# Optimization experiments

Hardware: AMD Instinct MI355X
Metric: run time of the kernel (lower is better)

## Reference

```python
import jax, jax.numpy as jnp
import numpy as np

NUM_HEADS = 8
EPS = 1e-12  # torch F.normalize default eps


def _l2_normalize(t, axis):
    n = jnp.sqrt(jnp.sum(t * t, axis=axis, keepdims=True))
    return t / jnp.maximum(n, EPS)


def setup_inputs() -> dict:
    key = jax.random.key(0)
    k1, k2, k3 = jax.random.split(key, 3)
    B, N, D = 32, 3136, 384
    x = jax.random.normal(k1, (B, N, D), dtype=jnp.float32)
    qkv_w = jax.random.normal(k2, (3 * D, D), dtype=jnp.float32) * (1.0 / np.sqrt(D))
    temperature = jnp.ones((NUM_HEADS, 1, 1), dtype=jnp.float32)
    proj_w = jax.random.normal(k3, (D, D), dtype=jnp.float32) * (1.0 / np.sqrt(D))
    proj_b = jnp.zeros((D,), dtype=jnp.float32)
    return {"x": x, "qkv_w": qkv_w, "temperature": temperature,
            "proj_w": proj_w, "proj_b": proj_b}


def reference(x, qkv_w, temperature, proj_w, proj_b):
    B, N, D = x.shape
    H = NUM_HEADS
    C = D // H
    # qkv projection (no bias), split last dim as (3, H, C) -> (3, B, H, C, N)
    qkv = jnp.einsum('bnd,ed->bne', x, qkv_w)
    qkv = qkv.reshape(B, N, 3, H, C).transpose(2, 0, 3, 4, 1)
    q, k, v = qkv[0], qkv[1], qkv[2]            # each (B, H, C, N)
    q = _l2_normalize(q, axis=-1)               # normalize over tokens N
    k = _l2_normalize(k, axis=-1)
    # cross-covariance attention: (B, H, C, C), scaled by per-head temperature
    attn = jnp.einsum('bhcn,bhdn->bhcd', q, k) * temperature
    attn = jax.nn.softmax(attn, axis=-1)
    out = jnp.einsum('bhcd,bhdn->bhcn', attn, v)  # (B, H, C, N)
    out = out.transpose(0, 3, 1, 2).reshape(B, N, D)
    return jnp.einsum('bnd,ed->bne', out, proj_w) + proj_b
```

## Files before the change

kernel.cpp:

```cpp
#include <hip/hip_runtime.h>


typedef __bf16 bf16x8 __attribute__((ext_vector_type(8)));
typedef float floatx4 __attribute__((ext_vector_type(4)));
typedef unsigned short u16;

#define B_ 32
#define N_ 3136
#define D_ 384
#define H_ 8
#define C_ 48
#define E3_ 1152
#define BN_ 100352

__device__ __forceinline__ u16 f2b(float f) {
  unsigned u = __builtin_bit_cast(unsigned, f);
  u += 0x7FFFu + ((u >> 16) & 1u);
  return (u16)(u >> 16);
}
__device__ __forceinline__ void gload16(const u16* g, u16* l) {
  __builtin_amdgcn_global_load_lds(
      (const __attribute__((address_space(1))) void*)g,
      (__attribute__((address_space(3))) void*)l, 16, 0, 0);
}

__global__ __launch_bounds__(256) void k_cvt(const float* __restrict__ in,
                                             u16* __restrict__ out, int n4) {
  int i = blockIdx.x * 256 + threadIdx.x;
  if (i < n4) {
    float4 v = ((const float4*)in)[i];
    ushort4 o;
    o.x = f2b(v.x); o.y = f2b(v.y); o.z = f2b(v.z); o.w = f2b(v.w);
    ((ushort4*)out)[i] = o;
  }
}

__global__ __launch_bounds__(256) void k_gemm_qkv(const u16* __restrict__ W,
                                                  const u16* __restrict__ X,
                                                  u16* __restrict__ O) {
  const int K = D_;
  int lin = blockIdx.y * 9 + blockIdx.x;
  int w = (lin & 7) * 882 + (lin >> 3);
  int m0 = (w % 9) * 128;
  int n0 = (w / 9) * 128;
  __shared__ u16 As[2][128][32];
  __shared__ u16 Bs[2][128][32];
  int t = threadIdx.x, wid = t >> 6, lane = t & 63;
  int srow = wid * 32 + (lane >> 2);
  int scol = (lane & 3) * 8;
  int wm = (wid & 1) * 64, wn = (wid >> 1) * 64;
  int r = lane & 15, quad = lane >> 4, q8 = quad * 8;

  const u16* gA = W + (size_t)(m0 + srow) * K + scol;
  const u16* gB = X + (size_t)(n0 + srow) * K + scol;

  floatx4 acc[4][4] = {};
  for (int k0 = 0; k0 < K; k0 += 64) {
#pragma unroll
    for (int ks = 0; ks < 2; ks++) {
      gload16(gA + k0 + ks * 32,          &As[ks][wid * 32][0]);
      gload16(gA + k0 + ks * 32 + 16 * K, &As[ks][wid * 32 + 16][0]);
      gload16(gB + k0 + ks * 32,          &Bs[ks][wid * 32][0]);
      gload16(gB + k0 + ks * 32 + 16 * K, &Bs[ks][wid * 32 + 16][0]);
    }
    __syncthreads();
#pragma unroll
    for (int ks = 0; ks < 2; ks++) {
      bf16x8 af[4], bf[4];
#pragma unroll
      for (int i = 0; i < 4; i++) af[i] = *(const bf16x8*)(&As[ks][wm + i * 16 + r][q8]);
#pragma unroll
      for (int j = 0; j < 4; j++) bf[j] = *(const bf16x8*)(&Bs[ks][wn + j * 16 + r][q8]);
#pragma unroll
      for (int i = 0; i < 4; i++)
#pragma unroll
        for (int j = 0; j < 4; j++)
          acc[i][j] = __builtin_amdgcn_mfma_f32_16x16x32_bf16(af[i], bf[j], acc[i][j], 0, 0, 0);
    }
    __syncthreads();
  }
#pragma unroll
  for (int i = 0; i < 4; i++)
#pragma unroll
    for (int j = 0; j < 4; j++)
#pragma unroll
      for (int v = 0; v < 4; v++) {
        int rr = m0 + wm + i * 16 + quad * 4 + v;
        int cc = n0 + wn + j * 16 + r;
        O[(size_t)rr * BN_ + cc] = f2b(acc[i][j][v]);
      }
}

__global__ __launch_bounds__(256) void k_attn_s(const u16* __restrict__ QKV,
                                                float* __restrict__ S,
                                                float* __restrict__ ssq) {
  int bh = blockIdx.x, b = bh >> 3, h = bh & 7;
  int ns = blockIdx.y * 448;
  const u16* Qb = QKV + (size_t)(h * C_) * BN_ + b * N_ + ns;
  const u16* Kb = QKV + (size_t)(D_ + h * C_) * BN_ + b * N_ + ns;
  __shared__ u16 As[64][32];
  __shared__ u16 Bs[64][32];
  int t = threadIdx.x, wid = t >> 6, lane = t & 63;
  int wm = (wid & 1) * 32, wn = (wid >> 1) * 32;
  int r = lane & 15, quad = lane >> 4, q8 = quad * 8;
  int srow = wid * 16 + (lane >> 2);
  int scol = (lane & 3) * 8;
  const u16* gQ = Qb + (size_t)srow * BN_ + scol;
  const u16* gK = Kb + (size_t)srow * BN_ + scol;
  u16* lQ = &As[wid * 16][0];
  u16* lK = &Bs[wid * 16][0];

  floatx4 acc[2][2] = {};
  floatx4 dq0 = {}, dq1 = {}, dk0 = {}, dk1 = {};
  for (int k0 = 0; k0 < 448; k0 += 32) {
    gload16(gQ + k0, lQ);
    gload16(gK + k0, lK);
    __syncthreads();
    bf16x8 a0 = *(const bf16x8*)(&As[wm + r][q8]);
    bf16x8 a1 = *(const bf16x8*)(&As[wm + 16 + r][q8]);
    bf16x8 b0 = *(const bf16x8*)(&Bs[wn + r][q8]);
    bf16x8 b1 = *(const bf16x8*)(&Bs[wn + 16 + r][q8]);
    acc[0][0] = __builtin_amdgcn_mfma_f32_16x16x32_bf16(a0, b0, acc[0][0], 0, 0, 0);
    acc[0][1] = __builtin_amdgcn_mfma_f32_16x16x32_bf16(a0, b1, acc[0][1], 0, 0, 0);
    acc[1][0] = __builtin_amdgcn_mfma_f32_16x16x32_bf16(a1, b0, acc[1][0], 0, 0, 0);
    acc[1][1] = __builtin_amdgcn_mfma_f32_16x16x32_bf16(a1, b1, acc[1][1], 0, 0, 0);
    if (wid == 0) {
      dq0 = __builtin_amdgcn_mfma_f32_16x16x32_bf16(a0, a0, dq0, 0, 0, 0);
      dq1 = __builtin_amdgcn_mfma_f32_16x16x32_bf16(a1, a1, dq1, 0, 0, 0);
      dk0 = __builtin_amdgcn_mfma_f32_16x16x32_bf16(b0, b0, dk0, 0, 0, 0);
      dk1 = __builtin_amdgcn_mfma_f32_16x16x32_bf16(b1, b1, dk1, 0, 0, 0);
    } else if (wid == 1) {
      dq0 = __builtin_amdgcn_mfma_f32_16x16x32_bf16(a0, a0, dq0, 0, 0, 0);
    } else if (wid == 2) {
      dk0 = __builtin_amdgcn_mfma_f32_16x16x32_bf16(b0, b0, dk0, 0, 0, 0);
    }
    __syncthreads();
  }
#pragma unroll
  for (int v = 0; v < 4; v++) {
    if (r == quad * 4 + v) {
      int dr = quad * 4 + v;
      if (wid == 0) {
        atomicAdd(&ssq[bh * 48 + dr],              dq0[v]);
        atomicAdd(&ssq[bh * 48 + 16 + dr],         dq1[v]);
        atomicAdd(&ssq[12288 + bh * 48 + dr],      dk0[v]);
        atomicAdd(&ssq[12288 + bh * 48 + 16 + dr], dk1[v]);
      } else if (wid == 1) {
        atomicAdd(&ssq[bh * 48 + 32 + dr], dq0[v]);
      } else if (wid == 2) {
        atomicAdd(&ssq[12288 + bh * 48 + 32 + dr], dk0[v]);
      }
    }
  }
#pragma unroll
  for (int mt = 0; mt < 2; mt++)
#pragma unroll
    for (int nt = 0; nt < 2; nt++)
#pragma unroll
      for (int v = 0; v < 4; v++) {
        int rr = wm + mt * 16 + quad * 4 + v;
        int cc = wn + nt * 16 + r;
        if (rr < 48 && cc < 48)
          atomicAdd(&S[(size_t)bh * 2304 + rr * 48 + cc], acc[mt][nt][v]);
      }
}

__global__ __launch_bounds__(64) void k_softmax(const float* __restrict__ S,
                                                const float* __restrict__ ssq,
                                                const float* __restrict__ temp,
                                                u16* __restrict__ attnb) {
  int bh = blockIdx.x, h = bh & 7;
  int c = threadIdx.x;
  if (c >= 48) return;
  float sq = 1.f / fmaxf(sqrtf(ssq[bh * 48 + c]), 1e-12f);
  float T = temp[h];
  const float* Srow = S + (size_t)bh * 2304 + c * 48;
  float v[48];
  float mx = -1e30f;
#pragma unroll
  for (int d = 0; d < 48; d++) {
    float sk = 1.f / fmaxf(sqrtf(ssq[12288 + bh * 48 + d]), 1e-12f);
    float l = Srow[d] * sq * sk * T;
    v[d] = l;
    mx = fmaxf(mx, l);
  }
  float sum = 0.f;
#pragma unroll
  for (int d = 0; d < 48; d++) { v[d] = expf(v[d] - mx); sum += v[d]; }
  float inv = 1.f / sum;
  u16* Arow = attnb + (size_t)bh * 3072 + c * 64;
#pragma unroll
  for (int d = 0; d < 48; d++) Arow[d] = f2b(v[d] * inv);
#pragma unroll
  for (int d = 48; d < 64; d++) Arow[d] = 0;
}

__global__ __launch_bounds__(256) void k_attn_v(const u16* __restrict__ QKV,
                                                const u16* __restrict__ attnb,
                                                u16* __restrict__ outT) {
  int bh = blockIdx.y, b = bh >> 3, h = bh & 7;
  int n0 = blockIdx.x * 64;
  const u16* V = QKV + (size_t)(2 * D_ + h * C_) * BN_ + b * N_;
  __shared__ u16 Vt[64][64];
  __shared__ u16 Aw[48][64];
  int t = threadIdx.x;
  for (int i = t; i < 512; i += 256) ((int4*)Vt)[i] = int4{0, 0, 0, 0};
  {
    const int4* src = (const int4*)(attnb + (size_t)bh * 3072);
    for (int i = t; i < 384; i += 256) ((int4*)Aw)[i] = src[i];
  }
  __syncthreads();
  for (int idx = t; idx < 768; idx += 256) {
    int d = idx >> 4, c4 = (idx & 15) * 4;
    ushort4 v = *(const ushort4*)(V + (size_t)d * BN_ + n0 + c4);
    Vt[c4 + 0][d] = v.x; Vt[c4 + 1][d] = v.y;
    Vt[c4 + 2][d] = v.z; Vt[c4 + 3][d] = v.w;
  }
  __syncthreads();
  int wid = t >> 6, lane = t & 63;
  int r = lane & 15, quad = lane >> 4, q8 = quad * 8;
  floatx4 acc[3] = {};
#pragma unroll
  for (int ks = 0; ks < 2; ks++) {
    bf16x8 a = *(const bf16x8*)(&Vt[wid * 16 + r][ks * 32 + q8]);
#pragma unroll
    for (int nt = 0; nt < 3; nt++) {
      bf16x8 bb = *(const bf16x8*)(&Aw[nt * 16 + r][ks * 32 + q8]);
      acc[nt] = __builtin_amdgcn_mfma_f32_16x16x32_bf16(a, bb, acc[nt], 0, 0, 0);
    }
  }
  u16* Ob = outT + (size_t)(b * N_) * D_;
#pragma unroll
  for (int nt = 0; nt < 3; nt++)
#pragma unroll
    for (int j = 0; j < 4; j++) {
      int n = n0 + wid * 16 + quad * 4 + j;
      int e = h * C_ + nt * 16 + r;
      Ob[(size_t)n * D_ + e] = f2b(acc[nt][j]);
    }
}

__global__ __launch_bounds__(256) void k_gemm_proj(const u16* __restrict__ OT,
                                                   const u16* __restrict__ P,
                                                   const float* __restrict__ bias,
                                                   float* __restrict__ Y) {
  const int K = D_;
  int lin = blockIdx.y * 3 + blockIdx.x;
  int w = (lin & 7) * 294 + (lin >> 3);
  int n0 = (w % 3) * 128;
  int m0 = (w / 3) * 128;
  __shared__ u16 As[2][128][32];
  __shared__ u16 Bs[2][128][32];
  int t = threadIdx.x, wid = t >> 6, lane = t & 63;
  int srow = wid * 32 + (lane >> 2);
  int scol = (lane & 3) * 8;
  int wm = (wid & 1) * 64, wn = (wid >> 1) * 64;
  int r = lane & 15, quad = lane >> 4, q8 = quad * 8;

  const u16* gA = OT + (size_t)(m0 + srow) * K + scol;
  const u16* gB = P + (size_t)(n0 + srow) * K + scol;

  floatx4 acc[4][4] = {};
  for (int k0 = 0; k0 < K; k0 += 64) {
#pragma unroll
    for (int ks = 0; ks < 2; ks++) {
      gload16(gA + k0 + ks * 32,          &As[ks][wid * 32][0]);
      gload16(gA + k0 + ks * 32 + 16 * K, &As[ks][wid * 32 + 16][0]);
      gload16(gB + k0 + ks * 32,          &Bs[ks][wid * 32][0]);
      gload16(gB + k0 + ks * 32 + 16 * K, &Bs[ks][wid * 32 + 16][0]);
    }
    __syncthreads();
#pragma unroll
    for (int ks = 0; ks < 2; ks++) {
      bf16x8 af[4], bf[4];
#pragma unroll
      for (int i = 0; i < 4; i++) af[i] = *(const bf16x8*)(&As[ks][wm + i * 16 + r][q8]);
#pragma unroll
      for (int j = 0; j < 4; j++) bf[j] = *(const bf16x8*)(&Bs[ks][wn + j * 16 + r][q8]);
#pragma unroll
      for (int i = 0; i < 4; i++)
#pragma unroll
        for (int j = 0; j < 4; j++)
          acc[i][j] = __builtin_amdgcn_mfma_f32_16x16x32_bf16(af[i], bf[j], acc[i][j], 0, 0, 0);
    }
    __syncthreads();
  }
#pragma unroll
  for (int i = 0; i < 4; i++)
#pragma unroll
    for (int j = 0; j < 4; j++) {
      int cc = n0 + wn + j * 16 + r;
      float bv = bias[cc];
#pragma unroll
      for (int v = 0; v < 4; v++) {
        int rr = m0 + wm + i * 16 + quad * 4 + v;
        Y[(size_t)rr * D_ + cc] = acc[i][j][v] + bv;
      }
    }
}

extern "C" void kernel_launch(void* const* d_in, const int* in_sizes, int n_in,
                              void* d_out, int out_size, void* d_ws, size_t ws_size,
                              hipStream_t stream) {
  const float* x      = (const float*)d_in[0];
  const float* qkv_w  = (const float*)d_in[1];
  const float* temp   = (const float*)d_in[2];
  const float* proj_w = (const float*)d_in[3];
  const float* proj_b = (const float*)d_in[4];
  float* out = (float*)d_out;

  char* ws = (char*)d_ws;
  u16*   qkv    = (u16*)(ws);
  u16*   xbf    = (u16*)(ws + 231211008);
  u16*   wbf    = (u16*)(ws + 308281344);
  u16*   pwbf   = (u16*)(ws + 309166080);
  float* S      = (float*)(ws + 309460992);
  float* ssq    = (float*)(ws + 311820288);
  u16*   attnb  = (u16*)(ws + 311918592);
  u16*   outT   = xbf;

  hipMemsetAsync(S, 0, 2359296 + 98304, stream);

  k_cvt<<<38535168 / 4 / 256, 256, 0, stream>>>(x, xbf, 38535168 / 4);
  k_cvt<<<442368 / 4 / 256, 256, 0, stream>>>(qkv_w, wbf, 442368 / 4);
  k_cvt<<<147456 / 4 / 256, 256, 0, stream>>>(proj_w, pwbf, 147456 / 4);

  k_gemm_qkv<<<dim3(9, 784), 256, 0, stream>>>(wbf, xbf, qkv);
  k_attn_s<<<dim3(256, 7), 256, 0, stream>>>(qkv, S, ssq);
  k_softmax<<<256, 64, 0, stream>>>(S, ssq, temp, attnb);
  k_attn_v<<<dim3(49, 256), 256, 0, stream>>>(qkv, attnb, outT);
  k_gemm_proj<<<dim3(3, 784), 256, 0, stream>>>(outT, pwbf, proj_b, out);
}
```

Baseline: 593.4 us.

## Reassociate attention via per-batch Gram matrix to avoid materializing QKV

Rewrites the pipeline algebraically: computes the per-batch Gram matrix X^T X (384x384) once. The q·k products and the q/k norms are then derived from W G W^T, and the value projection, attention and output projection are folded into one per-batch 384x384 matrix R that multiplies x directly. This drops the large QKV activation write and read, the per-head attention-v pass and the separate projection GEMM, at the cost of an extra transposed bf16 copy of x, fp32 atomic accumulation into G, and more bf16 rounding steps (G, U and R are each rounded to bf16).

Measured after the change: 557.6 us. 6.0% less time.

```diff
diff --git a/kernel.cpp b/kernel.cpp
--- a/kernel.cpp
+++ b/kernel.cpp
@@ -10,7 +10,6 @@
 #define D_ 384
 #define H_ 8
 #define C_ 48
-#define E3_ 1152
 #define BN_ 100352
 
 __device__ __forceinline__ u16 f2b(float f) {
@@ -35,33 +34,67 @@
   }
 }
 
-__global__ __launch_bounds__(256) void k_gemm_qkv(const u16* __restrict__ W,
-                                                  const u16* __restrict__ X,
-                                                  u16* __restrict__ O) {
-  const int K = D_;
-  int lin = blockIdx.y * 9 + blockIdx.x;
-  int w = (lin & 7) * 882 + (lin >> 3);
-  int m0 = (w % 9) * 128;
-  int n0 = (w / 9) * 128;
+__global__ __launch_bounds__(256) void k_cvt_t(const float* __restrict__ x,
+                                               u16* __restrict__ xbf,
+                                               u16* __restrict__ xT) {
+  int d0 = blockIdx.x * 64, n0 = blockIdx.y * 64, b = blockIdx.z;
+  const float* xp = x + ((size_t)b * N_ + n0) * D_ + d0;
+  __shared__ u16 L[64][68];
+  int t = threadIdx.x;
+  int nl = t >> 4, dl = (t & 15) * 4;
+#pragma unroll
+  for (int p = 0; p < 4; p++) {
+    int n = nl + p * 16;
+    float4 v = *(const float4*)(xp + (size_t)n * D_ + dl);
+    ushort4 o;
+    o.x = f2b(v.x); o.y = f2b(v.y); o.z = f2b(v.z); o.w = f2b(v.w);
+    *(ushort4*)(xbf + ((size_t)(b * N_ + n0 + n)) * D_ + d0 + dl) = o;
+    *(ushort4*)(&L[n][dl]) = o;
+  }
+  __syncthreads();
+  int dl2 = t >> 4, nl2 = (t & 15) * 4;
+#pragma unroll
+  for (int p = 0; p < 4; p++) {
+    int d = dl2 + p * 16;
+    ushort4 o;
+    o.x = L[nl2 + 0][d]; o.y = L[nl2 + 1][d];
+    o.z = L[nl2 + 2][d]; o.w = L[nl2 + 3][d];
+    *(ushort4*)(xT + (size_t)(d0 + d) * BN_ + b * N_ + n0 + nl2) = o;
+  }
+}
+
+__global__ __launch_bounds__(256) void k_wvt(const float* __restrict__ qkv_w,
+                                             u16* __restrict__ wvT) {
+  int h = blockIdx.x, t = threadIdx.x;
+  for (int idx = t; idx < 384 * 64; idx += 256) {
+    int j = idx >> 6, d = idx & 63;
+    float v = (d < 48) ? qkv_w[(size_t)(2 * D_ + h * C_ + d) * D_ + j] : 0.f;
+    wvT[(size_t)h * 24576 + idx] = f2b(v);
+  }
+}
+
+__global__ __launch_bounds__(256) void k_gram(const u16* __restrict__ xT,
+                                              float* __restrict__ G) {
+  int tile = blockIdx.x, b = blockIdx.y, ns = blockIdx.z * 448;
+  int m0 = (tile % 3) * 128, n0 = (tile / 3) * 128;
   __shared__ u16 As[2][128][32];
   __shared__ u16 Bs[2][128][32];
   int t = threadIdx.x, wid = t >> 6, lane = t & 63;
-  int srow = wid * 32 + (lane >> 2);
-  int scol = (lane & 3) * 8;
+  int srow = wid * 32 + (lane >> 2), scol = (lane & 3) * 8;
   int wm = (wid & 1) * 64, wn = (wid >> 1) * 64;
   int r = lane & 15, quad = lane >> 4, q8 = quad * 8;
-
-  const u16* gA = W + (size_t)(m0 + srow) * K + scol;
-  const u16* gB = X + (size_t)(n0 + srow) * K + scol;
+  const u16* base = xT + (size_t)b * N_ + ns + scol;
+  const u16* gA = base + (size_t)(m0 + srow) * BN_;
+  const u16* gB = base + (size_t)(n0 + srow) * BN_;
 
   floatx4 acc[4][4] = {};
-  for (int k0 = 0; k0 < K; k0 += 64) {
-#pragma unroll
-    for (int ks = 0; ks < 2; ks++) {
-      gload16(gA + k0 + ks * 32,          &As[ks][wid * 32][0]);
-      gload16(gA + k0 + ks * 32 + 16 * K, &As[ks][wid * 32 + 16][0]);
-      gload16(gB + k0 + ks * 32,          &Bs[ks][wid * 32][0]);
-      gload16(gB + k0 + ks * 32 + 16 * K, &Bs[ks][wid * 32 + 16][0]);
+  for (int k0 = 0; k0 < 448; k0 += 64) {
+#pragma unroll
+    for (int ks = 0; ks < 2; ks++) {
+      gload16(gA + k0 + ks * 32,                     &As[ks][wid * 32][0]);
+      gload16(gA + k0 + ks * 32 + (size_t)16 * BN_,  &As[ks][wid * 32 + 16][0]);
+      gload16(gB + k0 + ks * 32,                     &Bs[ks][wid * 32][0]);
+      gload16(gB + k0 + ks * 32 + (size_t)16 * BN_,  &Bs[ks][wid * 32 + 16][0]);
     }
     __syncthreads();
 #pragma unroll
@@ -79,6 +112,7 @@
     }
     __syncthreads();
   }
+  float* Gb = G + (size_t)b * 147456;
 #pragma unroll
   for (int i = 0; i < 4; i++)
 #pragma unroll
@@ -87,187 +121,31 @@
       for (int v = 0; v < 4; v++) {
         int rr = m0 + wm + i * 16 + quad * 4 + v;
         int cc = n0 + wn + j * 16 + r;
-        O[(size_t)rr * BN_ + cc] = f2b(acc[i][j][v]);
-      }
-}
-
-__global__ __launch_bounds__(256) void k_attn_s(const u16* __restrict__ QKV,
-                                                float* __restrict__ S,
-                                                float* __restrict__ ssq) {
-  int bh = blockIdx.x, b = bh >> 3, h = bh & 7;
-  int ns = blockIdx.y * 448;
-  const u16* Qb = QKV + (size_t)(h * C_) * BN_ + b * N_ + ns;
-  const u16* Kb = QKV + (size_t)(D_ + h * C_) * BN_ + b * N_ + ns;
-  __shared__ u16 As[64][32];
-  __shared__ u16 Bs[64][32];
-  int t = threadIdx.x, wid = t >> 6, lane = t & 63;
-  int wm = (wid & 1) * 32, wn = (wid >> 1) * 32;
-  int r = lane & 15, quad = lane >> 4, q8 = quad * 8;
-  int srow = wid * 16 + (lane >> 2);
-  int scol = (lane & 3) * 8;
-  const u16* gQ = Qb + (size_t)srow * BN_ + scol;
-  const u16* gK = Kb + (size_t)srow * BN_ + scol;
-  u16* lQ = &As[wid * 16][0];
-  u16* lK = &Bs[wid * 16][0];
-
-  floatx4 acc[2][2] = {};
-  floatx4 dq0 = {}, dq1 = {}, dk0 = {}, dk1 = {};
-  for (int k0 = 0; k0 < 448; k0 += 32) {
-    gload16(gQ + k0, lQ);
-    gload16(gK + k0, lK);
-    __syncthreads();
-    bf16x8 a0 = *(const bf16x8*)(&As[wm + r][q8]);
-    bf16x8 a1 = *(const bf16x8*)(&As[wm + 16 + r][q8]);
-    bf16x8 b0 = *(const bf16x8*)(&Bs[wn + r][q8]);
-    bf16x8 b1 = *(const bf16x8*)(&Bs[wn + 16 + r][q8]);
-    acc[0][0] = __builtin_amdgcn_mfma_f32_16x16x32_bf16(a0, b0, acc[0][0], 0, 0, 0);
-    acc[0][1] = __builtin_amdgcn_mfma_f32_16x16x32_bf16(a0, b1, acc[0][1], 0, 0, 0);
-    acc[1][0] = __builtin_amdgcn_mfma_f32_16x16x32_bf16(a1, b0, acc[1][0], 0, 0, 0);
-    acc[1][1] = __builtin_amdgcn_mfma_f32_16x16x32_bf16(a1, b1, acc[1][1], 0, 0, 0);
-    if (wid == 0) {
-      dq0 = __builtin_amdgcn_mfma_f32_16x16x32_bf16(a0, a0, dq0, 0, 0, 0);
-      dq1 = __builtin_amdgcn_mfma_f32_16x16x32_bf16(a1, a1, dq1, 0, 0, 0);
-      dk0 = __builtin_amdgcn_mfma_f32_16x16x32_bf16(b0, b0, dk0, 0, 0, 0);
-      dk1 = __builtin_amdgcn_mfma_f32_16x16x32_bf16(b1, b1, dk1, 0, 0, 0);
-    } else if (wid == 1) {
-      dq0 = __builtin_amdgcn_mfma_f32_16x16x32_bf16(a0, a0, dq0, 0, 0, 0);
-    } else if (wid == 2) {
-      dk0 = __builtin_amdgcn_mfma_f32_16x16x32_bf16(b0, b0, dk0, 0, 0, 0);
-    }
-    __syncthreads();
-  }
-#pragma unroll
-  for (int v = 0; v < 4; v++) {
-    if (r == quad * 4 + v) {
-      int dr = quad * 4 + v;
-      if (wid == 0) {
-        atomicAdd(&ssq[bh * 48 + dr],              dq0[v]);
-        atomicAdd(&ssq[bh * 48 + 16 + dr],         dq1[v]);
-        atomicAdd(&ssq[12288 + bh * 48 + dr],      dk0[v]);
-        atomicAdd(&ssq[12288 + bh * 48 + 16 + dr], dk1[v]);
-      } else if (wid == 1) {
-        atomicAdd(&ssq[bh * 48 + 32 + dr], dq0[v]);
-      } else if (wid == 2) {
-        atomicAdd(&ssq[12288 + bh * 48 + 32 + dr], dk0[v]);
-      }
-    }
-  }
-#pragma unroll
-  for (int mt = 0; mt < 2; mt++)
-#pragma unroll
-    for (int nt = 0; nt < 2; nt++)
-#pragma unroll
-      for (int v = 0; v < 4; v++) {
-        int rr = wm + mt * 16 + quad * 4 + v;
-        int cc = wn + nt * 16 + r;
-        if (rr < 48 && cc < 48)
-          atomicAdd(&S[(size_t)bh * 2304 + rr * 48 + cc], acc[mt][nt][v]);
-      }
-}
-
-__global__ __launch_bounds__(64) void k_softmax(const float* __restrict__ S,
-                                                const float* __restrict__ ssq,
-                                                const float* __restrict__ temp,
-                                                u16* __restrict__ attnb) {
-  int bh = blockIdx.x, h = bh & 7;
-  int c = threadIdx.x;
-  if (c >= 48) return;
-  float sq = 1.f / fmaxf(sqrtf(ssq[bh * 48 + c]), 1e-12f);
-  float T = temp[h];
-  const float* Srow = S + (size_t)bh * 2304 + c * 48;
-  float v[48];
-  float mx = -1e30f;
-#pragma unroll
-  for (int d = 0; d < 48; d++) {
-    float sk = 1.f / fmaxf(sqrtf(ssq[12288 + bh * 48 + d]), 1e-12f);
-    float l = Srow[d] * sq * sk * T;
-    v[d] = l;
-    mx = fmaxf(mx, l);
-  }
-  float sum = 0.f;
-#pragma unroll
-  for (int d = 0; d < 48; d++) { v[d] = expf(v[d] - mx); sum += v[d]; }
-  float inv = 1.f / sum;
-  u16* Arow = attnb + (size_t)bh * 3072 + c * 64;
-#pragma unroll
-  for (int d = 0; d < 48; d++) Arow[d] = f2b(v[d] * inv);
-#pragma unroll
-  for (int d = 48; d < 64; d++) Arow[d] = 0;
-}
-
-__global__ __launch_bounds__(256) void k_attn_v(const u16* __restrict__ QKV,
-                                                const u16* __restrict__ attnb,
-                                                u16* __restrict__ outT) {
-  int bh = blockIdx.y, b = bh >> 3, h = bh & 7;
-  int n0 = blockIdx.x * 64;
-  const u16* V = QKV + (size_t)(2 * D_ + h * C_) * BN_ + b * N_;
-  __shared__ u16 Vt[64][64];
-  __shared__ u16 Aw[48][64];
-  int t = threadIdx.x;
-  for (int i = t; i < 512; i += 256) ((int4*)Vt)[i] = int4{0, 0, 0, 0};
-  {
-    const int4* src = (const int4*)(attnb + (size_t)bh * 3072);
-    for (int i = t; i < 384; i += 256) ((int4*)Aw)[i] = src[i];
-  }
-  __syncthreads();
-  for (int idx = t; idx < 768; idx += 256) {
-    int d = idx >> 4, c4 = (idx & 15) * 4;
-    ushort4 v = *(const ushort4*)(V + (size_t)d * BN_ + n0 + c4);
-    Vt[c4 + 0][d] = v.x; Vt[c4 + 1][d] = v.y;
-    Vt[c4 + 2][d] = v.z; Vt[c4 + 3][d] = v.w;
-  }
-  __syncthreads();
-  int wid = t >> 6, lane = t & 63;
-  int r = lane & 15, quad = lane >> 4, q8 = quad * 8;
-  floatx4 acc[3] = {};
-#pragma unroll
-  for (int ks = 0; ks < 2; ks++) {
-    bf16x8 a = *(const bf16x8*)(&Vt[wid * 16 + r][ks * 32 + q8]);
-#pragma unroll
-    for (int nt = 0; nt < 3; nt++) {
-      bf16x8 bb = *(const bf16x8*)(&Aw[nt * 16 + r][ks * 32 + q8]);
-      acc[nt] = __builtin_amdgcn_mfma_f32_16x16x32_bf16(a, bb, acc[nt], 0, 0, 0);
-    }
-  }
-  u16* Ob = outT + (size_t)(b * N_) * D_;
-#pragma unroll
-  for (int nt = 0; nt < 3; nt++)
-#pragma unroll
-    for (int j = 0; j < 4; j++) {
-      int n = n0 + wid * 16 + quad * 4 + j;
-      int e = h * C_ + nt * 16 + r;
-      Ob[(size_t)n * D_ + e] = f2b(acc[nt][j]);
-    }
-}
-
-__global__ __launch_bounds__(256) void k_gemm_proj(const u16* __restrict__ OT,
-                                                   const u16* __restrict__ P,
-                                                   const float* __restrict__ bias,
-                                                   float* __restrict__ Y) {
-  const int K = D_;
-  int lin = blockIdx.y * 3 + blockIdx.x;
-  int w = (lin & 7) * 294 + (lin >> 3);
-  int n0 = (w % 3) * 128;
-  int m0 = (w / 3) * 128;
+        atomicAdd(&Gb[(size_t)rr * 384 + cc], acc[i][j][v]);
+      }
+}
+
+__global__ __launch_bounds__(256) void k_mid1(const u16* __restrict__ wbf,
+                                              const u16* __restrict__ Gb,
+                                              float* __restrict__ U) {
+  int m0 = blockIdx.x * 128, n0 = blockIdx.y * 128, b = blockIdx.z;
   __shared__ u16 As[2][128][32];
   __shared__ u16 Bs[2][128][32];
   int t = threadIdx.x, wid = t >> 6, lane = t & 63;
-  int srow = wid * 32 + (lane >> 2);
-  int scol = (lane & 3) * 8;
+  int srow = wid * 32 + (lane >> 2), scol = (lane & 3) * 8;
   int wm = (wid & 1) * 64, wn = (wid >> 1) * 64;
   int r = lane & 15, quad = lane >> 4, q8 = quad * 8;
-
-  const u16* gA = OT + (size_t)(m0 + srow) * K + scol;
-  const u16* gB = P + (size_t)(n0 + srow) * K + scol;
+  const u16* gA = wbf + (size_t)(m0 + srow) * 384 + scol;
+  const u16* gB = Gb + (size_t)b * 147456 + (size_t)(n0 + srow) * 384 + scol;
 
   floatx4 acc[4][4] = {};
-  for (int k0 = 0; k0 < K; k0 += 64) {
-#pragma unroll
-    for (int ks = 0; ks < 2; ks++) {
-      gload16(gA + k0 + ks * 32,          &As[ks][wid * 32][0]);
-      gload16(gA + k0 + ks * 32 + 16 * K, &As[ks][wid * 32 + 16][0]);
-      gload16(gB + k0 + ks * 32,          &Bs[ks][wid * 32][0]);
-      gload16(gB + k0 + ks * 32 + 16 * K, &Bs[ks][wid * 32 + 16][0]);
+  for (int k0 = 0; k0 < 384; k0 += 64) {
+#pragma unroll
+    for (int ks = 0; ks < 2; ks++) {
+      gload16(gA + k0 + ks * 32,            &As[ks][wid * 32][0]);
+      gload16(gA + k0 + ks * 32 + 16 * 384, &As[ks][wid * 32 + 16][0]);
+      gload16(gB + k0 + ks * 32,            &Bs[ks][wid * 32][0]);
+      gload16(gB + k0 + ks * 32 + 16 * 384, &Bs[ks][wid * 32 + 16][0]);
     }
     __syncthreads();
 #pragma unroll
@@ -285,16 +163,260 @@
     }
     __syncthreads();
   }
+  float* Ub = U + (size_t)b * 294912;
 #pragma unroll
   for (int i = 0; i < 4; i++)
 #pragma unroll
-    for (int j = 0; j < 4; j++) {
-      int cc = n0 + wn + j * 16 + r;
-      float bv = bias[cc];
+    for (int j = 0; j < 4; j++)
 #pragma unroll
       for (int v = 0; v < 4; v++) {
         int rr = m0 + wm + i * 16 + quad * 4 + v;
-        Y[(size_t)rr * D_ + cc] = acc[i][j][v] + bv;
+        int cc = n0 + wn + j * 16 + r;
+        Ub[(size_t)rr * 384 + cc] = acc[i][j][v];
+      }
+}
+
+__global__ __launch_bounds__(256) void k_mid2(const float* __restrict__ U,
+                                              const u16* __restrict__ wbf,
+                                              const u16* __restrict__ wvT,
+                                              const float* __restrict__ temp,
+                                              u16* __restrict__ MT) {
+  int bh = blockIdx.x, b = bh >> 3, h = bh & 7;
+  __shared__ __align__(16) u16 sUq[48][32], sUk[48][32], sWq[48][32], sWk[48][32];
+  __shared__ __align__(16) u16 sA[48][72];
+  __shared__ float sSsq[96];
+  __shared__ float sInv[96];
+  int t = threadIdx.x, wid = t >> 6, lane = t & 63;
+  int r = lane & 15, quad = lane >> 4, q8 = quad * 8;
+  const float* Uq = U + (size_t)b * 294912 + (size_t)(h * C_) * 384;
+  const float* Uk = U + (size_t)b * 294912 + (size_t)(D_ + h * C_) * 384;
+  const u16* Wq = wbf + (size_t)(h * C_) * 384;
+  const u16* Wk = wbf + (size_t)(D_ + h * C_) * 384;
+
+  floatx4 accS[3] = {};
+  floatx4 accD[6] = {};
+  for (int k0 = 0; k0 < 384; k0 += 32) {
+    for (int idx = t; idx < 768; idx += 256) {
+      int tile = idx / 192, rem = idx - tile * 192;
+      int rr = rem >> 2, c8 = (rem & 3) * 8;
+      if (tile < 2) {
+        const float* src = (tile == 0 ? Uq : Uk) + (size_t)rr * 384 + k0 + c8;
+        float4 a = *(const float4*)src;
+        float4 bb = *(const float4*)(src + 4);
+        ushort4 lo, hi;
+        lo.x = f2b(a.x); lo.y = f2b(a.y); lo.z = f2b(a.z); lo.w = f2b(a.w);
+        hi.x = f2b(bb.x); hi.y = f2b(bb.y); hi.z = f2b(bb.z); hi.w = f2b(bb.w);
+        u16* dst = (tile == 0 ? &sUq[rr][c8] : &sUk[rr][c8]);
+        *(ushort4*)dst = lo;
+        *(ushort4*)(dst + 4) = hi;
+      } else {
+        const u16* src = (tile == 2 ? Wq : Wk) + (size_t)rr * 384 + k0 + c8;
+        u16* dst = (tile == 2 ? &sWq[rr][c8] : &sWk[rr][c8]);
+        *(int4*)dst = *(const int4*)src;
+      }
+    }
+    __syncthreads();
+    if (wid < 3) {
+      bf16x8 uq = *(const bf16x8*)(&sUq[wid * 16 + r][q8]);
+#pragma unroll
+      for (int j = 0; j < 3; j++) {
+        bf16x8 wk = *(const bf16x8*)(&sWk[j * 16 + r][q8]);
+        accS[j] = __builtin_amdgcn_mfma_f32_16x16x32_bf16(uq, wk, accS[j], 0, 0, 0);
+      }
+    } else {
+#pragma unroll
+      for (int i = 0; i < 3; i++) {
+        bf16x8 uq = *(const bf16x8*)(&sUq[i * 16 + r][q8]);
+        bf16x8 wq = *(const bf16x8*)(&sWq[i * 16 + r][q8]);
+        bf16x8 uk = *(const bf16x8*)(&sUk[i * 16 + r][q8]);
+        bf16x8 wk = *(const bf16x8*)(&sWk[i * 16 + r][q8]);
+        accD[i]     = __builtin_amdgcn_mfma_f32_16x16x32_bf16(uq, wq, accD[i], 0, 0, 0);
+        accD[3 + i] = __builtin_amdgcn_mfma_f32_16x16x32_bf16(uk, wk, accD[3 + i], 0, 0, 0);
+      }
+    }
+    __syncthreads();
+  }
+  if (wid == 3) {
+#pragma unroll
+    for (int i = 0; i < 3; i++)
+#pragma unroll
+      for (int v = 0; v < 4; v++)
+        if (r == quad * 4 + v) {
+          sSsq[i * 16 + r] = accD[i][v];
+          sSsq[48 + i * 16 + r] = accD[3 + i][v];
+        }
+  }
+  __syncthreads();
+  if (t < 96) sInv[t] = 1.f / fmaxf(sqrtf(sSsq[t]), 1e-12f);
+  __syncthreads();
+  for (int idx = t; idx < 48 * 16; idx += 256) sA[idx >> 4][48 + (idx & 15)] = 0;
+  float T = temp[h];
+  if (wid < 3) {
+    float L[3][4];
+    int c_base = wid * 16 + quad * 4;
+#pragma unroll
+    for (int j = 0; j < 3; j++)
+#pragma unroll
+      for (int v = 0; v < 4; v++)
+        L[j][v] = accS[j][v] * sInv[c_base + v] * sInv[48 + j * 16 + r] * T;
+    float mx[4], sum[4];
+#pragma unroll
+    for (int v = 0; v < 4; v++) mx[v] = fmaxf(fmaxf(L[0][v], L[1][v]), L[2][v]);
+#pragma unroll
+    for (int m = 1; m <= 8; m <<= 1)
+#pragma unroll
+      for (int v = 0; v < 4; v++) mx[v] = fmaxf(mx[v], __shfl_xor(mx[v], m));
+#pragma unroll
+    for (int v = 0; v < 4; v++) sum[v] = 0.f;
+#pragma unroll
+    for (int j = 0; j < 3; j++)
+#pragma unroll
+      for (int v = 0; v < 4; v++) { L[j][v] = __expf(L[j][v] - mx[v]); sum[v] += L[j][v]; }
+#pragma unroll
+    for (int m = 1; m <= 8; m <<= 1)
+#pragma unroll
+      for (int v = 0; v < 4; v++) sum[v] += __shfl_xor(sum[v], m);
+#pragma unroll
+    for (int j = 0; j < 3; j++)
+#pragma unroll
+      for (int v = 0; v < 4; v++)
+        sA[c_base + v][j * 16 + r] = f2b(L[j][v] / sum[v]);
+  }
+  __syncthreads();
+  const u16* WvTh = wvT + (size_t)h * 24576;
+  floatx4 accM[3][6] = {};
+#pragma unroll
+  for (int ks = 0; ks < 2; ks++) {
+    bf16x8 af[3];
+#pragma unroll
+    for (int i = 0; i < 3; i++) af[i] = *(const bf16x8*)(&sA[i * 16 + r][ks * 32 + q8]);
+#pragma unroll
+    for (int jj = 0; jj < 6; jj++) {
+      int j = wid * 96 + jj * 16 + r;
+      bf16x8 bb = *(const bf16x8*)(WvTh + (size_t)j * 64 + ks * 32 + q8);
+#pragma unroll
+      for (int i = 0; i < 3; i++)
+        accM[i][jj] = __builtin_amdgcn_mfma_f32_16x16x32_bf16(af[i], bb, accM[i][jj], 0, 0, 0);
+    }
+  }
+  u16* MTb = MT + (size_t)b * 147456;
+#pragma unroll
+  for (int i = 0; i < 3; i++)
+#pragma unroll
+    for (int jj = 0; jj < 6; jj++)
+#pragma unroll
+      for (int v = 0; v < 4; v++) {
+        int c = i * 16 + quad * 4 + v;
+        int j = wid * 96 + jj * 16 + r;
+        MTb[(size_t)j * 384 + h * C_ + c] = f2b(accM[i][jj][v]);
+      }
+}
+
+__global__ __launch_bounds__(256) void k_mid3(const u16* __restrict__ pwbf,
+                                              const u16* __restrict__ MT,
+                                              u16* __restrict__ R) {
+  int m0 = (blockIdx.x % 3) * 128, n0 = (blockIdx.x / 3) * 128, b = blockIdx.y;
+  __shared__ u16 As[2][128][32];
+  __shared__ u16 Bs[2][128][32];
+  int t = threadIdx.x, wid = t >> 6, lane = t & 63;
+  int srow = wid * 32 + (lane >> 2), scol = (lane & 3) * 8;
+  int wm = (wid & 1) * 64, wn = (wid >> 1) * 64;
+  int r = lane & 15, quad = lane >> 4, q8 = quad * 8;
+  const u16* gA = pwbf + (size_t)(m0 + srow) * 384 + scol;
+  const u16* gB = MT + (size_t)b * 147456 + (size_t)(n0 + srow) * 384 + scol;
+
+  floatx4 acc[4][4] = {};
+  for (int k0 = 0; k0 < 384; k0 += 64) {
+#pragma unroll
+    for (int ks = 0; ks < 2; ks++) {
+      gload16(gA + k0 + ks * 32,            &As[ks][wid * 32][0]);
+      gload16(gA + k0 + ks * 32 + 16 * 384, &As[ks][wid * 32 + 16][0]);
+      gload16(gB + k0 + ks * 32,            &Bs[ks][wid * 32][0]);
+      gload16(gB + k0 + ks * 32 + 16 * 384, &Bs[ks][wid * 32 + 16][0]);
+    }
+    __syncthreads();
+#pragma unroll
+    for (int ks = 0; ks < 2; ks++) {
+      bf16x8 af[4], bf[4];
+#pragma unroll
+      for (int i = 0; i < 4; i++) af[i] = *(const bf16x8*)(&As[ks][wm + i * 16 + r][q8]);
+#pragma unroll
+      for (int j = 0; j < 4; j++) bf[j] = *(const bf16x8*)(&Bs[ks][wn + j * 16 + r][q8]);
+#pragma unroll
+      for (int i = 0; i < 4; i++)
+#pragma unroll
+        for (int j = 0; j < 4; j++)
+          acc[i][j] = __builtin_amdgcn_mfma_f32_16x16x32_bf16(af[i], bf[j], acc[i][j], 0, 0, 0);
+    }
+    __syncthreads();
+  }
+  u16* Rb = R + (size_t)b * 147456;
+#pragma unroll
+  for (int i = 0; i < 4; i++)
+#pragma unroll
+    for (int j = 0; j < 4; j++)
+#pragma unroll
+      for (int v = 0; v < 4; v++) {
+        int rr = m0 + wm + i * 16 + quad * 4 + v;
+        int cc = n0 + wn + j * 16 + r;
+        Rb[(size_t)rr * 384 + cc] = f2b(acc[i][j][v]);
+      }
+}
+
+__global__ __launch_bounds__(256) void k_final(const u16* __restrict__ xbf,
+                                               const u16* __restrict__ R,
+                                               const float* __restrict__ bias,
+                                               float* __restrict__ Y) {
+  int lin = blockIdx.y * 3 + blockIdx.x;
+  int w = (lin & 7) * 588 + (lin >> 3);
+  int ft = w % 3, gt = w / 3;
+  int b = gt / 49, n0 = (gt % 49) * 64;
+  size_t g0 = (size_t)b * N_ + n0;
+  int f0 = ft * 128;
+  __shared__ u16 As[2][64][32];
+  __shared__ u16 Bs[2][128][32];
+  int t = threadIdx.x, wid = t >> 6, lane = t & 63;
+  int srow = t >> 2, scol = (t & 3) * 8;
+  int wm = (wid & 1) * 32, wn = (wid >> 1) * 64;
+  int r = lane & 15, quad = lane >> 4, q8 = quad * 8;
+  const u16* gA = xbf + (g0 + srow) * 384 + scol;
+  const u16* gB1 = R + (size_t)b * 147456 + (size_t)(f0 + srow) * 384 + scol;
+  const u16* gB2 = gB1 + (size_t)64 * 384;
+
+  floatx4 acc[2][4] = {};
+  for (int k0 = 0; k0 < 384; k0 += 64) {
+#pragma unroll
+    for (int ks = 0; ks < 2; ks++) {
+      gload16(gA + k0 + ks * 32,  &As[ks][wid * 16][0]);
+      gload16(gB1 + k0 + ks * 32, &Bs[ks][wid * 16][0]);
+      gload16(gB2 + k0 + ks * 32, &Bs[ks][64 + wid * 16][0]);
+    }
+    __syncthreads();
+#pragma unroll
+    for (int ks = 0; ks < 2; ks++) {
+      bf16x8 af[2], bf[4];
+#pragma unroll
+      for (int i = 0; i < 2; i++) af[i] = *(const bf16x8*)(&As[ks][wm + i * 16 + r][q8]);
+#pragma unroll
+      for (int j = 0; j < 4; j++) bf[j] = *(const bf16x8*)(&Bs[ks][wn + j * 16 + r][q8]);
+#pragma unroll
+      for (int i = 0; i < 2; i++)
+#pragma unroll
+        for (int j = 0; j < 4; j++)
+          acc[i][j] = __builtin_amdgcn_mfma_f32_16x16x32_bf16(af[i], bf[j], acc[i][j], 0, 0, 0);
+    }
+    __syncthreads();
+  }
+#pragma unroll
+  for (int i = 0; i < 2; i++)
+#pragma unroll
+    for (int j = 0; j < 4; j++) {
+      int cc = wn + j * 16 + r;
+      float bv = bias[f0 + cc];
+#pragma unroll
+      for (int v = 0; v < 4; v++) {
+        int rr = wm + i * 16 + quad * 4 + v;
+        Y[(g0 + rr) * 384 + f0 + cc] = acc[i][j][v] + bv;
       }
     }
 }
@@ -310,24 +432,28 @@
   float* out = (float*)d_out;
 
   char* ws = (char*)d_ws;
-  u16*   qkv    = (u16*)(ws);
-  u16*   xbf    = (u16*)(ws + 231211008);
-  u16*   wbf    = (u16*)(ws + 308281344);
-  u16*   pwbf   = (u16*)(ws + 309166080);
-  float* S      = (float*)(ws + 309460992);
-  float* ssq    = (float*)(ws + 311820288);
-  u16*   attnb  = (u16*)(ws + 311918592);
-  u16*   outT   = xbf;
-
-  hipMemsetAsync(S, 0, 2359296 + 98304, stream);
-
-  k_cvt<<<38535168 / 4 / 256, 256, 0, stream>>>(x, xbf, 38535168 / 4);
-  k_cvt<<<442368 / 4 / 256, 256, 0, stream>>>(qkv_w, wbf, 442368 / 4);
-  k_cvt<<<147456 / 4 / 256, 256, 0, stream>>>(proj_w, pwbf, 147456 / 4);
-
-  k_gemm_qkv<<<dim3(9, 784), 256, 0, stream>>>(wbf, xbf, qkv);
-  k_attn_s<<<dim3(256, 7), 256, 0, stream>>>(qkv, S, ssq);
-  k_softmax<<<256, 64, 0, stream>>>(S, ssq, temp, attnb);
-  k_attn_v<<<dim3(49, 256), 256, 0, stream>>>(qkv, attnb, outT);
-  k_gemm_proj<<<dim3(3, 784), 256, 0, stream>>>(outT, pwbf, proj_b, out);
-}
+  u16*   xbf  = (u16*)(ws);
+  u16*   xT   = (u16*)(ws + 77070336);
+  u16*   wbf  = (u16*)(ws + 154140672);
+  u16*   pwbf = (u16*)(ws + 155025408);
+  u16*   wvT  = (u16*)(ws + 155320320);
+  float* G    = (float*)(ws + 155713536);
+  u16*   Gbf  = (u16*)(ws + 174587904);
+  float* U    = (float*)(ws + 184025088);
+  u16*   MT   = (u16*)(ws + 221773824);
+  u16*   R    = (u16*)(ws + 231211008);
+
+  hipMemsetAsync(G, 0, 18874368, stream);
+
+  k_cvt_t<<<dim3(6, 49, 32), 256, 0, stream>>>(x, xbf, xT);
+  k_cvt<<<432, 256, 0, stream>>>(qkv_w, wbf, 110592);
+  k_cvt<<<144, 256, 0, stream>>>(proj_w, pwbf, 36864);
+  k_wvt<<<8, 256, 0, stream>>>(qkv_w, wvT);
+
+  k_gram<<<dim3(9, 32, 7), 256, 0, stream>>>(xT, G);
+  k_cvt<<<4608, 256, 0, stream>>>(G, Gbf, 1179648);
+  k_mid1<<<dim3(6, 3, 32), 256, 0, stream>>>(wbf, Gbf, U);
+  k_mid2<<<256, 256, 0, stream>>>(U, wbf, wvT, temp, MT);
+  k_mid3<<<dim3(9, 32), 256, 0, stream>>>(pwbf, MT, R);
+  k_final<<<dim3(3, 1568), 256, 0, stream>>>(xbf, R, proj_b, out);
+}
```
